# Performance work log

Hardware: AMD Instinct MI355X
Metric: run time of the kernel (lower is better)

The kernel has to match this reference:

```python
import jax, jax.numpy as jnp
import numpy as np

NEG_SLOPE = 0.2  # PyG GATConv default negative_slope


def gat_conv(x, edge_index, W, att_src, att_dst, bias, concat):
    """PyG-style GATConv (eval mode, add_self_loops=True).
    W: [in, H*C]; att_src/att_dst: [H, C]; bias: [H*C] or [C]."""
    N = x.shape[0]
    H, C = att_src.shape
    loop = jnp.arange(N, dtype=edge_index.dtype)
    src = jnp.concatenate([edge_index[0], loop])  # message sources
    dst = jnp.concatenate([edge_index[1], loop])  # aggregation targets
    h = (x @ W).reshape(N, H, C)                  # [N, H, C]
    a_s = jnp.einsum('nhc,hc->nh', h, att_src)    # [N, H]
    a_d = jnp.einsum('nhc,hc->nh', h, att_dst)
    e = jax.nn.leaky_relu(a_s[src] + a_d[dst], NEG_SLOPE)  # [E, H]
    # segment softmax over incoming edges of each destination node
    m = jax.ops.segment_max(e, dst, num_segments=N)
    ex = jnp.exp(e - m[dst])
    denom = jax.ops.segment_sum(ex, dst, num_segments=N)
    alpha = ex / (denom[dst] + 1e-16)             # [E, H]
    out = jax.ops.segment_sum(h[src] * alpha[:, :, None], dst, num_segments=N)
    out = out.reshape(N, H * C) if concat else out.mean(axis=1)
    return out + bias


def setup_inputs() -> dict:
    key = jax.random.key(0)
    ks = jax.random.split(key, 13)
    N, E, G = 100000, 3200000, 512
    IN, HID, HEADS, OUT = 1, 8, 8, 10
    p = lambda k, shape: jax.random.normal(k, shape, jnp.float32) * 0.1
    return {
        'x': jax.random.normal(ks[0], (N, IN), jnp.float32),
        'edge_index': jax.random.randint(ks[1], (2, E), 0, N),
        'batch': jnp.sort(jax.random.randint(ks[2], (N,), 0, G)),
        'num_graphs': G,
        'W1': p(ks[3], (IN, HEADS * HID)),
        'att_src1': p(ks[4], (HEADS, HID)),
        'att_dst1': p(ks[5], (HEADS, HID)),
        'b1': jnp.zeros((HEADS * HID,), jnp.float32),
        'W2': p(ks[6], (HEADS * HID, HID)),
        'att_src2': p(ks[7], (1, HID)),
        'att_dst2': p(ks[8], (1, HID)),
        'b2': jnp.zeros((HID,), jnp.float32),
        'lin_w': p(ks[9], (HID, OUT)),
        'lin_b': jnp.zeros((OUT,), jnp.float32),
    }


def reference(x, edge_index, batch, num_graphs, W1, att_src1, att_dst1, b1,
              W2, att_src2, att_dst2, b2, lin_w, lin_b):
    # eval mode: F.dropout is identity
    h = gat_conv(x, edge_index, W1, att_src1, att_dst1, b1, concat=True)   # [N, 64]
    h = jax.nn.elu(h)
    h = gat_conv(h, edge_index, W2, att_src2, att_dst2, b2, concat=False)  # [N, 8]
    # global mean pool over graphs
    sums = jax.ops.segment_sum(h, batch, num_segments=num_graphs)
    cnt = jax.ops.segment_sum(jnp.ones((h.shape[0], 1), h.dtype), batch,
                              num_segments=num_graphs)
    pooled = sums / jnp.maximum(cnt, 1.0)                                   # [G, 8]
    logits = pooled @ lin_w + lin_b                                         # [G, 10]
    return jax.nn.log_softmax(logits, axis=1)
```

## Files before the change

### kernel.cpp

```cpp
#include <hip/hip_runtime.h>
#include <hip/hip_bf16.h>

#define NEG 0.2f
#define NBMAX 512
#define BCAP 12288
#define TILE 12500
#define EPT 13

__global__ void __launch_bounds__(1024) kP_bucket(
    const int* __restrict__ src, const int* __restrict__ dst,
    int* __restrict__ gcur, unsigned int* __restrict__ packed, int E, int NB)
{
    __shared__ int hist[NBMAX], lofs[NBMAX], gbase[NBMAX], cur[NBMAX];
    __shared__ int wtot[8], wpre[8];
    __shared__ unsigned int stage[TILE];
    int tid = threadIdx.x;
    int lane = tid & 63, wv = tid >> 6;
    if (tid < NBMAX) hist[tid] = 0;
    __syncthreads();
    int t0 = blockIdx.x * TILE;
    int tend = t0 + TILE; if (tend > E) tend = E;
    int dreg[EPT];
    #pragma unroll
    for (int k = 0; k < EPT; ++k) {
        int i = t0 + tid + (k << 10);
        int d = -1;
        if (i < tend) { d = dst[i]; atomicAdd(&hist[d >> 8], 1); }
        dreg[k] = d;
    }
    __syncthreads();
    int v = (tid < NBMAX) ? hist[tid] : 0;
    int incl = v;
    #pragma unroll
    for (int off = 1; off < 64; off <<= 1) {
        int t = __shfl_up(incl, off, 64);
        if (lane >= off) incl += t;
    }
    if (tid < NBMAX && lane == 63) wtot[wv] = incl;
    __syncthreads();
    if (tid == 0) { int p = 0; for (int i = 0; i < 8; ++i) { wpre[i] = p; p += wtot[i]; } }
    __syncthreads();
    if (tid < NBMAX) {
        lofs[tid] = wpre[wv] + incl - v;
        gbase[tid] = v ? atomicAdd(&gcur[tid], v) : 0;
        cur[tid] = 0;
    }
    __syncthreads();
    #pragma unroll
    for (int k = 0; k < EPT; ++k) {
        int d = dreg[k];
        if (d >= 0) {
            int i = t0 + tid + (k << 10);
            int j = d >> 8;
            int pos = lofs[j] + atomicAdd(&cur[j], 1);
            stage[pos] = ((unsigned)src[i] << 8) | (unsigned)(d & 255);
        }
    }
    __syncthreads();
    int sg = lane >> 5, sl = lane & 31;
    for (int j = wv * 2 + sg; j < NB; j += 32) {
        int h = hist[j];
        if (!h) continue;
        int lo = lofs[j], gb = gbase[j];
        for (int k = sl; k < h; k += 32) {
            int gp = gb + k;
            if (gp < BCAP) packed[(size_t)j * BCAP + gp] = stage[lo + k];
        }
    }
}

__global__ void __launch_bounds__(512) kL1(
    const int* __restrict__ gcur, unsigned int* packed,
    const float* __restrict__ x,
    const float* __restrict__ W1, const float* __restrict__ as1, const float* __restrict__ ad1,
    const float* __restrict__ b1, const float* __restrict__ W2,
    const float* __restrict__ as2w, const float* __restrict__ ad2w,
    const int* __restrict__ batch, int* __restrict__ gstart,
    int* __restrict__ rowS, int* __restrict__ rowE,
    float* __restrict__ h2, float* __restrict__ as2, float* __restrict__ ad2, int N, int G)
{
    __shared__ int hist[256], roff[256], cur[256];
    __shared__ int stage[BCAP];
    __shared__ float S1[8], D1[8], sW1[64], sb1[64], sW2[512], sas[8], sad[8];
    int tid = threadIdx.x, b = blockIdx.x;
    if (tid < 8) {
        float sv = 0.f, dv = 0.f;
        for (int c = 0; c < 8; ++c) {
            float w = W1[tid * 8 + c];
            sv += w * as1[tid * 8 + c];
            dv += w * ad1[tid * 8 + c];
        }
        S1[tid] = sv; D1[tid] = dv;
        sas[tid] = as2w[tid]; sad[tid] = ad2w[tid];
    }
    for (int i = tid; i < 64; i += 512) { sW1[i] = W1[i]; sb1[i] = b1[i]; }
    if (tid < 512) sW2[tid] = W2[tid];
    if (tid < 256) hist[tid] = 0;
    if (tid < 256) {
        int node = b * 256 + tid;
        if (node < N) {
            int b0 = batch[node];
            if (node == 0) { for (int g = 0; g <= b0; ++g) gstart[g] = 0; }
            else { int bp = batch[node - 1]; for (int g = bp + 1; g <= b0; ++g) gstart[g] = node; }
            if (node == N - 1) { for (int g = b0 + 1; g <= G; ++g) gstart[g] = N; }
        }
    }
    __syncthreads();
    int cnt = gcur[b]; if (cnt > BCAP) cnt = BCAP;
    size_t base = (size_t)b * BCAP;
    unsigned int* pk = packed + base;
    for (int i = tid; i < cnt; i += 512)
        atomicAdd(&hist[pk[i] & 255], 1);
    __syncthreads();
    int v = (tid < 256) ? hist[tid] : 0;
    if (tid < 256) roff[tid] = v;
    __syncthreads();
    for (int off = 1; off < 256; off <<= 1) {
        int t = (tid >= off && tid < 256) ? roff[tid - off] : 0;
        __syncthreads();
        if (tid < 256) roff[tid] += t;
        __syncthreads();
    }
    if (tid < 256) cur[tid] = roff[tid] - v;
    __syncthreads();
    for (int i = tid; i < cnt; i += 512) {
        unsigned p = pk[i];
        int pos = atomicAdd(&cur[p & 255], 1);
        stage[pos] = (int)(p >> 8);
    }
    __syncthreads();
    for (int i = tid; i < cnt; i += 512)
        pk[i] = (unsigned)stage[i];
    int nl = tid >> 1, sub = tid & 1;
    int node = b * 256 + nl;
    bool valid = node < N;
    int en = roff[nl], st = en - hist[nl];
    if (valid && sub == 0) { rowS[node] = (int)base + st; rowE[node] = (int)base + en; }
    float xdv = valid ? x[node] : 0.f;
    float s1r[8], d1r[8];
    #pragma unroll
    for (int h = 0; h < 8; ++h) { s1r[h] = S1[h]; d1r[h] = D1[h]; }
    float num[8] = {0,0,0,0,0,0,0,0}, den[8] = {0,0,0,0,0,0,0,0};
    if (valid && sub == 0) {
        #pragma unroll
        for (int h = 0; h < 8; ++h) {
            float e = xdv * (s1r[h] + d1r[h]);
            e = fmaxf(e, NEG * e);
            float w = __expf(e);
            den[h] = w; num[h] = w * xdv;
        }
    }
    for (int j = st + sub; j < en; j += 2) {
        float xsv = x[stage[j]];
        #pragma unroll
        for (int h = 0; h < 8; ++h) {
            float e = xsv * s1r[h] + xdv * d1r[h];
            e = fmaxf(e, NEG * e);
            float w = __expf(e);
            den[h] += w; num[h] += w * xsv;
        }
    }
    #pragma unroll
    for (int h = 0; h < 8; ++h) {
        den[h] += __shfl_xor(den[h], 1, 64);
        num[h] += __shfl_xor(num[h], 1, 64);
    }
    if (!valid || sub) return;
    float o[8] = {0,0,0,0,0,0,0,0};
    #pragma unroll
    for (int h = 0; h < 8; ++h) {
        float agg = num[h] / (den[h] + 1e-16f);
        #pragma unroll
        for (int c = 0; c < 8; ++c) {
            float vv = agg * sW1[h * 8 + c] + sb1[h * 8 + c];
            vv = vv > 0.f ? vv : (__expf(vv) - 1.f);
            #pragma unroll
            for (int c2 = 0; c2 < 8; ++c2) o[c2] += vv * sW2[(h * 8 + c) * 8 + c2];
        }
    }
    float as_ = 0.f, ad_ = 0.f;
    #pragma unroll
    for (int c = 0; c < 8; ++c) {
        as_ += o[c] * sas[c];
        ad_ += o[c] * sad[c];
        h2[(size_t)node * 8 + c] = o[c];
    }
    as2[node] = as_; ad2[node] = ad_;
}

__global__ void __launch_bounds__(256) kG2_gather(
    const int* __restrict__ rowS, const int* __restrict__ rowE,
    const unsigned int* __restrict__ csr,
    const float* __restrict__ as2, const float* __restrict__ ad2,
    const float* __restrict__ h2,
    float* __restrict__ out2, int N)
{
    int t = blockIdx.x * blockDim.x + threadIdx.x;
    int node = t >> 3, lane = t & 7;
    if (node >= N) return;
    float add = ad2[node];
    float den = 0.f, num[8] = {0,0,0,0,0,0,0,0};
    if (lane == 0) {
        float e = as2[node] + add;
        e = fmaxf(e, NEG * e);
        float w = __expf(e);
        den = w;
        const float4* hp = (const float4*)&h2[(size_t)node * 8];
        float4 a = hp[0], b = hp[1];
        num[0] = w * a.x; num[1] = w * a.y; num[2] = w * a.z; num[3] = w * a.w;
        num[4] = w * b.x; num[5] = w * b.y; num[6] = w * b.z; num[7] = w * b.w;
    }
    int start = rowS[node], end = rowE[node];
    for (int j = start + lane; j < end; j += 8) {
        int s = (int)csr[j];
        float e = as2[s] + add;
        e = fmaxf(e, NEG * e);
        float w = __expf(e);
        den += w;
        const float4* hp = (const float4*)&h2[(size_t)s * 8];
        float4 a = hp[0], b = hp[1];
        num[0] += w * a.x; num[1] += w * a.y; num[2] += w * a.z; num[3] += w * a.w;
        num[4] += w * b.x; num[5] += w * b.y; num[6] += w * b.z; num[7] += w * b.w;
    }
    #pragma unroll
    for (int off = 4; off >= 1; off >>= 1) {
        den += __shfl_down(den, off, 8);
        #pragma unroll
        for (int c = 0; c < 8; ++c) num[c] += __shfl_down(num[c], off, 8);
    }
    if (lane == 0) {
        float dv = den + 1e-16f;
        #pragma unroll
        for (int c = 0; c < 8; ++c) out2[(size_t)node * 8 + c] = num[c] / dv;
    }
}

__global__ void __launch_bounds__(256) kPool(
    const float* __restrict__ out2, const int* __restrict__ gstart,
    const float* __restrict__ b2v,
    const float* __restrict__ lin_w, const float* __restrict__ lin_b,
    float* __restrict__ out, int G)
{
    __shared__ float sw[80], sb[10], sb2[8];
    if (threadIdx.x < 80) sw[threadIdx.x] = lin_w[threadIdx.x];
    if (threadIdx.x < 10) sb[threadIdx.x] = lin_b[threadIdx.x];
    if (threadIdx.x < 8)  sb2[threadIdx.x] = b2v[threadIdx.x];
    __syncthreads();
    int wid = (blockIdx.x * blockDim.x + threadIdx.x) >> 6;
    if (wid >= G) return;
    int lane = threadIdx.x & 63;
    int ch = lane & 7, sub = lane >> 3;
    int start = gstart[wid], end = gstart[wid + 1];
    int cntn = end - start;
    float acc = 0.f;
    for (int i = start + sub; i < end; i += 8)
        acc += out2[(size_t)i * 8 + ch];
    acc += __shfl_down(acc, 32, 64);
    acc += __shfl_down(acc, 16, 64);
    acc += __shfl_down(acc, 8, 64);
    float inv = (cntn > 0) ? 1.f / (float)cntn : 0.f;
    float p[8];
    #pragma unroll
    for (int i = 0; i < 8; ++i) {
        float tt = __shfl(acc, i, 64);
        p[i] = (cntn > 0) ? (tt * inv + sb2[i]) : 0.f;
    }
    float l[10]; float m = -1e30f;
    #pragma unroll
    for (int j = 0; j < 10; ++j) {
        float v = sb[j];
        #pragma unroll
        for (int i = 0; i < 8; ++i) v += p[i] * sw[i * 10 + j];
        l[j] = v; m = v > m ? v : m;
    }
    float sum = 0.f;
    #pragma unroll
    for (int j = 0; j < 10; ++j) sum += __expf(l[j] - m);
    float lse = m + __logf(sum);
    if (lane < 10) out[(size_t)wid * 10 + lane] = l[lane] - lse;
}

extern "C" void kernel_launch(void* const* d_in, const int* in_sizes, int n_in,
                              void* d_out, int out_size, void* d_ws, size_t ws_size,
                              hipStream_t stream) {
    const float* x    = (const float*)d_in[0];
    const int*   ei   = (const int*)d_in[1];
    const int*   batch= (const int*)d_in[2];
    const float* W1   = (const float*)d_in[4];
    const float* as1  = (const float*)d_in[5];
    const float* ad1  = (const float*)d_in[6];
    const float* b1   = (const float*)d_in[7];
    const float* W2   = (const float*)d_in[8];
    const float* as2w = (const float*)d_in[9];
    const float* ad2w = (const float*)d_in[10];
    const float* b2v  = (const float*)d_in[11];
    const float* lw   = (const float*)d_in[12];
    const float* lb   = (const float*)d_in[13];
    float* out = (float*)d_out;

    const int N = in_sizes[0];
    const int E = in_sizes[1] / 2;
    const int G = out_size / 10;
    const int* srcI = ei;
    const int* dstI = ei + E;
    const int NB = (N + 255) >> 8;

    int*   gcur = (int*)d_ws;
    unsigned int* packed = (unsigned int*)(gcur + 512);
    int*   rowS = (int*)(packed + (size_t)NB * BCAP);
    int*   rowE = rowS + N;
    float* h2   = (float*)(rowE + N);
    float* as2  = h2 + (size_t)8 * N;
    float* ad2  = as2 + N;
    float* out2 = ad2 + N;
    int*   gstart = (int*)(out2 + (size_t)8 * N);

    const int B = 256;
    hipMemsetAsync(gcur, 0, 512 * sizeof(int), stream);

    kP_bucket<<<(E + TILE - 1) / TILE, 1024, 0, stream>>>(srcI, dstI, gcur, packed, E, NB);
    kL1<<<NB, 512, 0, stream>>>(gcur, packed, x, W1, as1, ad1, b1, W2, as2w, ad2w,
                                batch, gstart, rowS, rowE, h2, as2, ad2, N, G);
    kG2_gather<<<(N * 8 + B - 1) / B, B, 0, stream>>>(rowS, rowE, packed, as2, ad2, h2,
                                                      out2, N);
    kPool<<<(G * 64 + B - 1) / B, B, 0, stream>>>(out2, gstart, b2v, lw, lb, out, G);
}
```

Before: 199.2 us.

## Pack layer-2 features with source attention score, unroll gathers, wave-shuffle scan

Interleaves each node's 8 hidden features and its source attention logit into one 12-float record, so the layer-2 edge gather reads one contiguous region instead of two separate arrays. The gather and layer-1 edge loops are unrolled by two to keep more independent loads in flight. The 256-entry block prefix scan is replaced by wavefront shuffle scans plus a small cross-wave combine, cutting barrier count. The padded record raises per-node footprint from 9 to 12 floats.

```diff
diff --git a/kernel.cpp b/kernel.cpp
--- a/kernel.cpp
+++ b/kernel.cpp
@@ -77,12 +77,14 @@
     const float* __restrict__ as2w, const float* __restrict__ ad2w,
     const int* __restrict__ batch, int* __restrict__ gstart,
     int* __restrict__ rowS, int* __restrict__ rowE,
-    float* __restrict__ h2, float* __restrict__ as2, float* __restrict__ ad2, int N, int G)
+    float* __restrict__ rec, float* __restrict__ ad2, int N, int G)
 {
     __shared__ int hist[256], roff[256], cur[256];
     __shared__ int stage[BCAP];
+    __shared__ int wtot[4], wpre[4];
     __shared__ float S1[8], D1[8], sW1[64], sb1[64], sW2[512], sas[8], sad[8];
     int tid = threadIdx.x, b = blockIdx.x;
+    int lane = tid & 63, wv = tid >> 6;
     if (tid < 8) {
         float sv = 0.f, dv = 0.f;
         for (int c = 0; c < 8; ++c) {
@@ -112,16 +114,24 @@
     for (int i = tid; i < cnt; i += 512)
         atomicAdd(&hist[pk[i] & 255], 1);
     __syncthreads();
-    int v = (tid < 256) ? hist[tid] : 0;
-    if (tid < 256) roff[tid] = v;
-    __syncthreads();
-    for (int off = 1; off < 256; off <<= 1) {
-        int t = (tid >= off && tid < 256) ? roff[tid - off] : 0;
-        __syncthreads();
-        if (tid < 256) roff[tid] += t;
-        __syncthreads();
-    }
-    if (tid < 256) cur[tid] = roff[tid] - v;
+    int v = 0, incl = 0;
+    if (tid < 256) {
+        v = hist[tid];
+        incl = v;
+        #pragma unroll
+        for (int off = 1; off < 64; off <<= 1) {
+            int t = __shfl_up(incl, off, 64);
+            if (lane >= off) incl += t;
+        }
+        if (lane == 63) wtot[wv] = incl;
+    }
+    __syncthreads();
+    if (tid == 0) { int p = 0; for (int i = 0; i < 4; ++i) { wpre[i] = p; p += wtot[i]; } }
+    __syncthreads();
+    if (tid < 256) {
+        roff[tid] = wpre[wv] + incl;
+        cur[tid] = wpre[wv] + incl - v;
+    }
     __syncthreads();
     for (int i = tid; i < cnt; i += 512) {
         unsigned p = pk[i];
@@ -150,7 +160,22 @@
             den[h] = w; num[h] = w * xdv;
         }
     }
-    for (int j = st + sub; j < en; j += 2) {
+    int j = st + sub;
+    for (; j + 2 < en; j += 4) {
+        float xa = x[stage[j]];
+        float xb = x[stage[j + 2]];
+        #pragma unroll
+        for (int h = 0; h < 8; ++h) {
+            float ea = xa * s1r[h] + xdv * d1r[h];
+            float eb = xb * s1r[h] + xdv * d1r[h];
+            ea = fmaxf(ea, NEG * ea);
+            eb = fmaxf(eb, NEG * eb);
+            float wa = __expf(ea), wb = __expf(eb);
+            den[h] += wa + wb;
+            num[h] += wa * xa + wb * xb;
+        }
+    }
+    for (; j < en; j += 2) {
         float xsv = x[stage[j]];
         #pragma unroll
         for (int h = 0; h < 8; ++h) {
@@ -179,20 +204,21 @@
         }
     }
     float as_ = 0.f, ad_ = 0.f;
+    float* rp = rec + (size_t)node * 12;
     #pragma unroll
     for (int c = 0; c < 8; ++c) {
         as_ += o[c] * sas[c];
         ad_ += o[c] * sad[c];
-        h2[(size_t)node * 8 + c] = o[c];
-    }
-    as2[node] = as_; ad2[node] = ad_;
+        rp[c] = o[c];
+    }
+    rp[8] = as_;
+    ad2[node] = ad_;
 }
 
 __global__ void __launch_bounds__(256) kG2_gather(
     const int* __restrict__ rowS, const int* __restrict__ rowE,
     const unsigned int* __restrict__ csr,
-    const float* __restrict__ as2, const float* __restrict__ ad2,
-    const float* __restrict__ h2,
+    const float* __restrict__ rec, const float* __restrict__ ad2,
     float* __restrict__ out2, int N)
 {
     int t = blockIdx.x * blockDim.x + threadIdx.x;
@@ -201,24 +227,45 @@
     float add = ad2[node];
     float den = 0.f, num[8] = {0,0,0,0,0,0,0,0};
     if (lane == 0) {
-        float e = as2[node] + add;
+        const float* rp = rec + (size_t)node * 12;
+        float e = rp[8] + add;
         e = fmaxf(e, NEG * e);
         float w = __expf(e);
         den = w;
-        const float4* hp = (const float4*)&h2[(size_t)node * 8];
+        const float4* hp = (const float4*)rp;
         float4 a = hp[0], b = hp[1];
         num[0] = w * a.x; num[1] = w * a.y; num[2] = w * a.z; num[3] = w * a.w;
         num[4] = w * b.x; num[5] = w * b.y; num[6] = w * b.z; num[7] = w * b.w;
     }
     int start = rowS[node], end = rowE[node];
-    for (int j = start + lane; j < end; j += 8) {
+    int j = start + lane;
+    for (; j + 8 < end; j += 16) {
+        int s0 = (int)csr[j], s1 = (int)csr[j + 8];
+        const float* r0 = rec + (size_t)s0 * 12;
+        const float* r1 = rec + (size_t)s1 * 12;
+        const float4* h0 = (const float4*)r0;
+        const float4* h1 = (const float4*)r1;
+        float4 a0 = h0[0], b0 = h0[1];
+        float4 a1 = h1[0], b1 = h1[1];
+        float e0 = r0[8] + add, e1 = r1[8] + add;
+        e0 = fmaxf(e0, NEG * e0);
+        e1 = fmaxf(e1, NEG * e1);
+        float w0 = __expf(e0), w1 = __expf(e1);
+        den += w0 + w1;
+        num[0] += w0 * a0.x + w1 * a1.x; num[1] += w0 * a0.y + w1 * a1.y;
+        num[2] += w0 * a0.z + w1 * a1.z; num[3] += w0 * a0.w + w1 * a1.w;
+        num[4] += w0 * b0.x + w1 * b1.x; num[5] += w0 * b0.y + w1 * b1.y;
+        num[6] += w0 * b0.z + w1 * b1.z; num[7] += w0 * b0.w + w1 * b1.w;
+    }
+    for (; j < end; j += 8) {
         int s = (int)csr[j];
-        float e = as2[s] + add;
+        const float* rp = rec + (size_t)s * 12;
+        const float4* hp = (const float4*)rp;
+        float4 a = hp[0], b = hp[1];
+        float e = rp[8] + add;
         e = fmaxf(e, NEG * e);
         float w = __expf(e);
         den += w;
-        const float4* hp = (const float4*)&h2[(size_t)s * 8];
-        float4 a = hp[0], b = hp[1];
         num[0] += w * a.x; num[1] += w * a.y; num[2] += w * a.z; num[3] += w * a.w;
         num[4] += w * b.x; num[5] += w * b.y; num[6] += w * b.z; num[7] += w * b.w;
     }
@@ -309,9 +356,8 @@
     unsigned int* packed = (unsigned int*)(gcur + 512);
     int*   rowS = (int*)(packed + (size_t)NB * BCAP);
     int*   rowE = rowS + N;
-    float* h2   = (float*)(rowE + N);
-    float* as2  = h2 + (size_t)8 * N;
-    float* ad2  = as2 + N;
+    float* rec  = (float*)(rowE + N);
+    float* ad2  = rec + (size_t)12 * N;
     float* out2 = ad2 + N;
     int*   gstart = (int*)(out2 + (size_t)8 * N);
 
@@ -320,8 +366,8 @@
 
     kP_bucket<<<(E + TILE - 1) / TILE, 1024, 0, stream>>>(srcI, dstI, gcur, packed, E, NB);
     kL1<<<NB, 512, 0, stream>>>(gcur, packed, x, W1, as1, ad1, b1, W2, as2w, ad2w,
-                                batch, gstart, rowS, rowE, h2, as2, ad2, N, G);
-    kG2_gather<<<(N * 8 + B - 1) / B, B, 0, stream>>>(rowS, rowE, packed, as2, ad2, h2,
+                                batch, gstart, rowS, rowE, rec, ad2, N, G);
+    kG2_gather<<<(N * 8 + B - 1) / B, B, 0, stream>>>(rowS, rowE, packed, rec, ad2,
                                                       out2, N);
     kPool<<<(G * 64 + B - 1) / B, B, 0, stream>>>(out2, gstart, b2v, lw, lb, out, G);
 }
```

Result: no change. 201.7 us (+1.3%).
